# Performance work log

Measured on AMD Instinct MI355X. Metric: run time of the kernel, lower is better.

Reference implementation:

```python
import jax, jax.numpy as jnp
import numpy as np

MAX_LEVELS = 5
CHANNELS = 3


def _gauss_kernel(channels=CHANNELS):
    k = np.array([[1., 4., 6., 4., 1.],
                  [4., 16., 24., 16., 4.],
                  [6., 24., 36., 24., 6.],
                  [4., 16., 24., 16., 4.],
                  [1., 4., 6., 4., 1.]], dtype=np.float32) / 256.0
    return jnp.asarray(np.tile(k[None, None], (channels, 1, 1, 1)))  # (C,1,5,5)


def conv_gauss(img, kernel):
    # reflect-pad by 2 then depthwise 5x5 conv (groups = C)
    img = jnp.pad(img, ((0, 0), (0, 0), (2, 2), (2, 2)), mode='reflect')
    return jax.lax.conv_general_dilated(
        img, kernel, window_strides=(1, 1), padding='VALID',
        dimension_numbers=('NCHW', 'OIHW', 'NCHW'),
        feature_group_count=img.shape[1])


def downsample(x):
    return x[:, :, ::2, ::2]


def upsample(x, kernel):
    # zero-stuff: x at even (h,w) positions, zeros elsewhere, then smooth with 4*kernel
    b, c, h, w = x.shape
    up = jnp.zeros((b, c, 2 * h, 2 * w), dtype=x.dtype).at[:, :, ::2, ::2].set(x)
    return conv_gauss(up, 4.0 * kernel)


def laplacian_pyramid(img, kernel, max_levels=MAX_LEVELS):
    current = img
    pyr = []
    for _ in range(max_levels):
        filtered = conv_gauss(current, kernel)
        down = downsample(filtered)
        up = upsample(down, kernel)
        pyr.append(current - up)
        current = down
    return pyr


def setup_inputs() -> dict:
    key = jax.random.key(0)
    k1, k2 = jax.random.split(key)
    shape = (32, 3, 512, 512)
    return {
        'input': jax.random.normal(k1, shape, dtype=jnp.float32),
        'target': jax.random.normal(k2, shape, dtype=jnp.float32),
        'kernel': _gauss_kernel(CHANNELS),
    }


def reference(input, target, kernel):
    pyr_in = laplacian_pyramid(input, kernel, MAX_LEVELS)
    pyr_tg = laplacian_pyramid(target, kernel, MAX_LEVELS)
    # F.l1_loss default reduction: mean over all elements, per level
    return sum(jnp.mean(jnp.abs(a - b)) for a, b in zip(pyr_in, pyr_tg))
```

## Files before the change

kernel.cpp:

```cpp
#include <hip/hip_runtime.h>


#define BC 96
#define KA 0.0625f
#define KB 0.25f
#define KC 0.375f

__device__ __forceinline__ int refl(int i, int n) {
    if (i < 0) i = -i;
    if (i >= n) i = 2 * n - 2 - i;
    return i;
}

template<int H, int NC, bool DIFF>
__device__ __forceinline__ void load_raw(const float* __restrict__ pa,
                                         const float* __restrict__ pb,
                                         int r, int basec,
                                         float* __restrict__ a,
                                         float* __restrict__ b) {
    const int off = r * H + basec;
    if constexpr (NC == 8) {
        float4 a0 = *(const float4*)(pa + off);
        float4 a1 = *(const float4*)(pa + off + 4);
        a[0]=a0.x; a[1]=a0.y; a[2]=a0.z; a[3]=a0.w;
        a[4]=a1.x; a[5]=a1.y; a[6]=a1.z; a[7]=a1.w;
        if constexpr (DIFF) {
            float4 b0 = *(const float4*)(pb + off);
            float4 b1 = *(const float4*)(pb + off + 4);
            b[0]=b0.x; b[1]=b0.y; b[2]=b0.z; b[3]=b0.w;
            b[4]=b1.x; b[5]=b1.y; b[6]=b1.z; b[7]=b1.w;
        }
    } else if constexpr (NC == 4) {
        float4 a0 = *(const float4*)(pa + off);
        a[0]=a0.x; a[1]=a0.y; a[2]=a0.z; a[3]=a0.w;
        if constexpr (DIFF) {
            float4 b0 = *(const float4*)(pb + off);
            b[0]=b0.x; b[1]=b0.y; b[2]=b0.z; b[3]=b0.w;
        }
    } else {
        float2 a0 = *(const float2*)(pa + off);
        a[0]=a0.x; a[1]=a0.y;
        if constexpr (DIFF) {
            float2 b0 = *(const float2*)(pb + off);
            b[0]=b0.x; b[1]=b0.y;
        }
    }
}

template<int NC, bool DIFF>
__device__ __forceinline__ void materialize(const float* __restrict__ a,
                                            const float* __restrict__ b,
                                            float* __restrict__ c) {
#pragma unroll
    for (int i = 0; i < NC; ++i) c[i] = DIFF ? (a[i] - b[i]) : a[i];
}

template<int NC>
__device__ __forceinline__ void hconv(const float* __restrict__ c,
                                      float* __restrict__ o, int lane) {
    constexpr int ND = NC / 2;
    float e[NC + 3];
#pragma unroll
    for (int i = 0; i < NC; ++i) e[i + 2] = c[i];
    const bool l0 = (lane == 0), l63 = (lane == 63);
    { float v = __shfl(e[NC + 1], lane - 1); e[1] = l0 ? e[3] : v; }
    if constexpr (NC >= 4) {
        { float v = __shfl(e[NC], lane - 1); e[0] = l0 ? e[4] : v; }
        { float v = __shfl(e[2], lane + 1); e[NC + 2] = l63 ? e[NC] : v; }
    } else {
        e[0] = __shfl(e[2], l0 ? 1 : lane - 1);
        e[NC + 2] = __shfl(e[2], l63 ? 63 : lane + 1);
    }
#pragma unroll
    for (int j = 0; j < ND; ++j)
        o[j] = KA * e[2*j] + KB * e[2*j+1] + KC * e[2*j+2]
             + KB * e[2*j+3] + KA * e[2*j+4];
}

template<int H, int NC, bool DIFF, int R>
__global__ __launch_bounds__(256) void lap_slide(
        const float* __restrict__ A, const float* __restrict__ B,
        float* __restrict__ down, float* __restrict__ out, float invN) {
    constexpr int Hd = H / 2, ND = NC / 2, SPP = H / R;
    __shared__ float red[4];
    const int tid = threadIdx.x;
    const int lane = tid & 63, wid = tid >> 6;
    const int sid = blockIdx.x * 4 + wid;
    const int bc = sid / SPP;
    const int y0 = (sid % SPP) * R;
    const float* pa = A + (size_t)bc * H * H;
    const float* pb = DIFF ? (B + (size_t)bc * H * H) : nullptr;
    float* pd = down + (size_t)bc * Hd * Hd;
    const int basec = lane * NC;

    float h0[ND], h1[ND], h2[ND], h3[ND], h4[ND];
    float w0[NC], w1[NC], w2[NC];
    float eOld[NC], eMid[NC], oPrev[NC];
    float nA1[NC], nB1[NC], nA2[NC], nB2[NC];
    float c1[NC], c2[NC], t[NC], tb[NC];
#pragma unroll
    for (int i = 0; i < NC; ++i) {
        w0[i] = 0.f; w1[i] = 0.f; w2[i] = 0.f;
        eOld[i] = 0.f; oPrev[i] = 0.f;
    }
    float acc = 0.f;

    const int d0 = y0 >> 1;
    int dbeg = d0 - 1; if (dbeg < 0) dbeg = 0;
    const int dend = d0 + R / 2;

    load_raw<H,NC,DIFF>(pa, pb, refl(2*dbeg - 2, H), basec, t, tb);
    materialize<NC,DIFF>(t, tb, c1); hconv<NC>(c1, h0, lane);
    load_raw<H,NC,DIFF>(pa, pb, refl(2*dbeg - 1, H), basec, t, tb);
    materialize<NC,DIFF>(t, tb, c1); hconv<NC>(c1, h1, lane);
    load_raw<H,NC,DIFF>(pa, pb, refl(2*dbeg, H), basec, t, tb);
    materialize<NC,DIFF>(t, tb, eMid); hconv<NC>(eMid, h2, lane);
    load_raw<H,NC,DIFF>(pa, pb, refl(2*dbeg + 1, H), basec, nA1, nB1);
    load_raw<H,NC,DIFF>(pa, pb, refl(2*dbeg + 2, H), basec, nA2, nB2);

    for (int d = dbeg; d <= dend; ++d) {
        materialize<NC,DIFF>(nA1, nB1, c1);
        materialize<NC,DIFF>(nA2, nB2, c2);
        load_raw<H,NC,DIFF>(pa, pb, refl(2*d + 3, H), basec, nA1, nB1);
        load_raw<H,NC,DIFF>(pa, pb, refl(2*d + 4, H), basec, nA2, nB2);

        hconv<NC>(c1, h3, lane);
        hconv<NC>(c2, h4, lane);

        float dn[ND];
#pragma unroll
        for (int j = 0; j < ND; ++j)
            dn[j] = KA*h0[j] + KB*h1[j] + KC*h2[j] + KB*h3[j] + KA*h4[j];

        if (d >= d0 && d < d0 + R/2) {
            const int doff = d * Hd + lane * ND;
            if constexpr (ND == 4) {
                float4 s; s.x=dn[0]; s.y=dn[1]; s.z=dn[2]; s.w=dn[3];
                *(float4*)(pd + doff) = s;
            } else if constexpr (ND == 2) {
                float2 s; s.x=dn[0]; s.y=dn[1];
                *(float2*)(pd + doff) = s;
            } else {
                pd[doff] = dn[0];
            }
        }

        float dm, dp;
        if constexpr (ND >= 2) {
            { float v = __shfl(dn[ND-1], lane - 1); dm = (lane == 0)  ? dn[1]    : v; }
            { float v = __shfl(dn[0],    lane + 1); dp = (lane == 63) ? dn[ND-1] : v; }
        } else {
            dm = __shfl(dn[0], (lane == 0)  ? 1  : lane - 1);
            dp = __shfl(dn[0], (lane == 63) ? 63 : lane + 1);
        }
#pragma unroll
        for (int i = 0; i < NC; ++i) { w0[i] = w1[i]; w1[i] = w2[i]; }
#pragma unroll
        for (int j = 0; j < ND; ++j) {
            float lf = j ? dn[j-1] : dm;
            float rg = (j + 1 < ND) ? dn[j+1] : dp;
            w2[2*j]     = 0.125f * lf + 0.75f * dn[j] + 0.125f * rg;
            w2[2*j + 1] = 0.5f * (dn[j] + rg);
        }

        if (d >= d0 + 1) {
            const int ye = 2 * d - 2;
            if (ye == 0) {
#pragma unroll
                for (int i = 0; i < NC; ++i) {
                    acc += fabsf(eOld[i]  - (0.75f*w1[i] + 0.25f*w2[i]));
                    acc += fabsf(oPrev[i] - 0.5f*(w1[i] + w2[i]));
                }
            } else if (ye == H - 2) {
#pragma unroll
                for (int i = 0; i < NC; ++i) {
                    acc += fabsf(eOld[i]  - (0.125f*w0[i] + 0.875f*w1[i]));
                    acc += fabsf(oPrev[i] - w1[i]);
                }
            } else {
#pragma unroll
                for (int i = 0; i < NC; ++i) {
                    acc += fabsf(eOld[i]  - (0.125f*w0[i] + 0.75f*w1[i] + 0.125f*w2[i]));
                    acc += fabsf(oPrev[i] - 0.5f*(w1[i] + w2[i]));
                }
            }
        }

#pragma unroll
        for (int i = 0; i < NC; ++i) {
            eOld[i] = eMid[i]; eMid[i] = c2[i]; oPrev[i] = c1[i];
        }
#pragma unroll
        for (int j = 0; j < ND; ++j) { h0[j] = h2[j]; h1[j] = h3[j]; h2[j] = h4[j]; }
    }

#pragma unroll
    for (int off2 = 32; off2 > 0; off2 >>= 1)
        acc += __shfl_down(acc, off2, 64);
    if (lane == 0) red[wid] = acc;
    __syncthreads();
    if (tid == 0)
        atomicAdd(out, (red[0] + red[1] + red[2] + red[3]) * invN);
}

__global__ __launch_bounds__(1024) void lap_small(
        const float* __restrict__ dsrc, float* __restrict__ out,
        float invN3, float invN4) {
    __shared__ float p[64 * 66];
    __shared__ float hh[64 * 34];
    __shared__ float dd[32 * 34];
    __shared__ float W3[32 * 64];
    __shared__ float h4[32 * 18];
    __shared__ float d4[16 * 18];
    __shared__ float W4[16 * 32];
    __shared__ float red[16];
    const int tid = threadIdx.x;
    const float* src = dsrc + (size_t)blockIdx.x * 4096;
    for (int i = tid; i < 4096; i += 1024)
        p[(i >> 6) * 66 + (i & 63)] = src[i];
    __syncthreads();
    const float k[5] = {KA, KB, KC, KB, KA};
    for (int i = tid; i < 64 * 32; i += 1024) {
        int r = i >> 5, t = i & 31;
        const float* pr = p + r * 66;
        float s = 0.f;
#pragma unroll
        for (int v = 0; v < 5; ++v) s += k[v] * pr[refl(2*t + v - 2, 64)];
        hh[r * 34 + t] = s;
    }
    __syncthreads();
    for (int i = tid; i < 32 * 32; i += 1024) {
        int dy = i >> 5, t = i & 31;
        float s = 0.f;
#pragma unroll
        for (int u = 0; u < 5; ++u) s += k[u] * hh[refl(2*dy + u - 2, 64) * 34 + t];
        dd[dy * 34 + t] = s;
    }
    __syncthreads();
    for (int i = tid; i < 32 * 32; i += 1024) {
        int a = i >> 5, t = i & 31;
        const float* dr = dd + a * 34;
        float dm = dr[t == 0 ? 1 : t - 1];
        float dc = dr[t];
        float dp = dr[t == 31 ? 31 : t + 1];
        W3[a * 64 + 2*t]     = 0.125f * dm + 0.75f * dc + 0.125f * dp;
        W3[a * 64 + 2*t + 1] = 0.5f * (dc + dp);
    }
    __syncthreads();
    float acc3 = 0.f;
    for (int i = tid; i < 4096; i += 1024) {
        int y = i >> 6, x = i & 63;
        float cur = p[y * 66 + x];
        float up;
        if ((y & 1) == 0) {
            int a0 = refl(y - 2, 64) >> 1, a1 = y >> 1, a2 = refl(y + 2, 64) >> 1;
            up = 0.125f*W3[a0*64 + x] + 0.75f*W3[a1*64 + x] + 0.125f*W3[a2*64 + x];
        } else {
            int a0 = (y - 1) >> 1, a1 = refl(y + 1, 64) >> 1;
            up = 0.5f * (W3[a0*64 + x] + W3[a1*64 + x]);
        }
        acc3 += fabsf(cur - up);
    }
    __syncthreads();
    for (int i = tid; i < 32 * 16; i += 1024) {
        int r = i >> 4, t = i & 15;
        const float* pr = dd + r * 34;
        float s = 0.f;
#pragma unroll
        for (int v = 0; v < 5; ++v) s += k[v] * pr[refl(2*t + v - 2, 32)];
        h4[r * 18 + t] = s;
    }
    __syncthreads();
    for (int i = tid; i < 16 * 16; i += 1024) {
        int dy = i >> 4, t = i & 15;
        float s = 0.f;
#pragma unroll
        for (int u = 0; u < 5; ++u) s += k[u] * h4[refl(2*dy + u - 2, 32) * 18 + t];
        d4[dy * 18 + t] = s;
    }
    __syncthreads();
    for (int i = tid; i < 16 * 16; i += 1024) {
        int a = i >> 4, t = i & 15;
        const float* dr = d4 + a * 18;
        float dm = dr[t == 0 ? 1 : t - 1];
        float dc = dr[t];
        float dp = dr[t == 15 ? 15 : t + 1];
        W4[a * 32 + 2*t]     = 0.125f * dm + 0.75f * dc + 0.125f * dp;
        W4[a * 32 + 2*t + 1] = 0.5f * (dc + dp);
    }
    __syncthreads();
    float acc4 = 0.f;
    for (int i = tid; i < 1024; i += 1024) {
        int y = i >> 5, x = i & 31;
        float cur = dd[y * 34 + x];
        float up;
        if ((y & 1) == 0) {
            int a0 = refl(y - 2, 32) >> 1, a1 = y >> 1, a2 = refl(y + 2, 32) >> 1;
            up = 0.125f*W4[a0*32 + x] + 0.75f*W4[a1*32 + x] + 0.125f*W4[a2*32 + x];
        } else {
            int a0 = (y - 1) >> 1, a1 = refl(y + 1, 32) >> 1;
            up = 0.5f * (W4[a0*32 + x] + W4[a1*32 + x]);
        }
        acc4 += fabsf(cur - up);
    }
    float acc = acc3 * invN3 + acc4 * invN4;
#pragma unroll
    for (int off2 = 32; off2 > 0; off2 >>= 1)
        acc += __shfl_down(acc, off2, 64);
    int lane = tid & 63, wid = tid >> 6;
    if (lane == 0) red[wid] = acc;
    __syncthreads();
    if (tid == 0) {
        float s = 0.f;
#pragma unroll
        for (int i = 0; i < 16; ++i) s += red[i];
        atomicAdd(out, s);
    }
}

extern "C" void kernel_launch(void* const* d_in, const int* in_sizes, int n_in,
                              void* d_out, int out_size, void* d_ws, size_t ws_size,
                              hipStream_t stream) {
    const float* in = (const float*)d_in[0];
    const float* tg = (const float*)d_in[1];
    float* out = (float*)d_out;
    float* ws = (float*)d_ws;

    float* down0 = ws;
    float* down1 = down0 + (size_t)BC * 256 * 256;
    float* down2 = down1 + (size_t)BC * 128 * 128;

    hipMemsetAsync(out, 0, sizeof(float), stream);

    lap_slide<512, 8, true, 16><<<96 * 32 / 4, 256, 0, stream>>>(
        in, tg, down0, out, 1.f / (96.f * 512.f * 512.f));
    lap_slide<256, 4, false, 8><<<96 * 32 / 4, 256, 0, stream>>>(
        down0, nullptr, down1, out, 1.f / (96.f * 256.f * 256.f));
    lap_slide<128, 2, false, 4><<<96 * 32 / 4, 256, 0, stream>>>(
        down1, nullptr, down2, out, 1.f / (96.f * 128.f * 128.f));
    lap_small<<<BC, 1024, 0, stream>>>(
        down2, out, 1.f / (96.f * 64.f * 64.f), 1.f / (96.f * 32.f * 32.f));
}
```

Baseline: 263.4 us.

## Fold partial upsample terms into running residuals to cut registers; raise occupancy

The sliding-window state is restructured: instead of keeping three rows of horizontal upsample values plus the even/odd source rows, the kernel pre-subtracts each row's contribution into running residuals (pA, pB, pC), so fewer live arrays are carried between iterations. Launch bounds now request 8 blocks per CU, and the first level uses half the rows per wave with twice the grid. This aims to lower register pressure and raise occupancy and parallelism, at the cost of more halo reloads per strip and some reordering of floating-point sums.

New measurement: 522.2 us. +98.3%, slower.

```diff
diff --git a/kernel.cpp b/kernel.cpp
--- a/kernel.cpp
+++ b/kernel.cpp
@@ -78,7 +78,7 @@
 }
 
 template<int H, int NC, bool DIFF, int R>
-__global__ __launch_bounds__(256) void lap_slide(
+__global__ __launch_bounds__(256, 8) void lap_slide(
         const float* __restrict__ A, const float* __restrict__ B,
         float* __restrict__ down, float* __restrict__ out, float invN) {
     constexpr int Hd = H / 2, ND = NC / 2, SPP = H / R;
@@ -94,14 +94,12 @@
     const int basec = lane * NC;
 
     float h0[ND], h1[ND], h2[ND], h3[ND], h4[ND];
-    float w0[NC], w1[NC], w2[NC];
-    float eOld[NC], eMid[NC], oPrev[NC];
+    float wPrev[NC], pA[NC], pB[NC], pC[NC];
     float nA1[NC], nB1[NC], nA2[NC], nB2[NC];
     float c1[NC], c2[NC], t[NC], tb[NC];
 #pragma unroll
     for (int i = 0; i < NC; ++i) {
-        w0[i] = 0.f; w1[i] = 0.f; w2[i] = 0.f;
-        eOld[i] = 0.f; oPrev[i] = 0.f;
+        wPrev[i] = 0.f; pA[i] = 0.f; pB[i] = 0.f; pC[i] = 0.f;
     }
     float acc = 0.f;
 
@@ -114,7 +112,11 @@
     load_raw<H,NC,DIFF>(pa, pb, refl(2*dbeg - 1, H), basec, t, tb);
     materialize<NC,DIFF>(t, tb, c1); hconv<NC>(c1, h1, lane);
     load_raw<H,NC,DIFF>(pa, pb, refl(2*dbeg, H), basec, t, tb);
-    materialize<NC,DIFF>(t, tb, eMid); hconv<NC>(eMid, h2, lane);
+    materialize<NC,DIFF>(t, tb, c2); hconv<NC>(c2, h2, lane);
+    if (d0 == 0) {
+#pragma unroll
+        for (int i = 0; i < NC; ++i) pC[i] = c2[i];
+    }
     load_raw<H,NC,DIFF>(pa, pb, refl(2*dbeg + 1, H), basec, nA1, nB1);
     load_raw<H,NC,DIFF>(pa, pb, refl(2*dbeg + 2, H), basec, nA2, nB2);
 
@@ -153,14 +155,13 @@
             dm = __shfl(dn[0], (lane == 0)  ? 1  : lane - 1);
             dp = __shfl(dn[0], (lane == 63) ? 63 : lane + 1);
         }
-#pragma unroll
-        for (int i = 0; i < NC; ++i) { w0[i] = w1[i]; w1[i] = w2[i]; }
+        float wN[NC];
 #pragma unroll
         for (int j = 0; j < ND; ++j) {
             float lf = j ? dn[j-1] : dm;
             float rg = (j + 1 < ND) ? dn[j+1] : dp;
-            w2[2*j]     = 0.125f * lf + 0.75f * dn[j] + 0.125f * rg;
-            w2[2*j + 1] = 0.5f * (dn[j] + rg);
+            wN[2*j]     = 0.125f * lf + 0.75f * dn[j] + 0.125f * rg;
+            wN[2*j + 1] = 0.5f * (dn[j] + rg);
         }
 
         if (d >= d0 + 1) {
@@ -168,27 +169,30 @@
             if (ye == 0) {
 #pragma unroll
                 for (int i = 0; i < NC; ++i) {
-                    acc += fabsf(eOld[i]  - (0.75f*w1[i] + 0.25f*w2[i]));
-                    acc += fabsf(oPrev[i] - 0.5f*(w1[i] + w2[i]));
+                    acc += fabsf(pA[i] - (0.75f*wPrev[i] + 0.25f*wN[i]));
+                    acc += fabsf(pB[i] - 0.5f*wN[i]);
                 }
             } else if (ye == H - 2) {
 #pragma unroll
                 for (int i = 0; i < NC; ++i) {
-                    acc += fabsf(eOld[i]  - (0.125f*w0[i] + 0.875f*w1[i]));
-                    acc += fabsf(oPrev[i] - w1[i]);
+                    acc += fabsf(pA[i] - 0.875f*wPrev[i]);
+                    acc += fabsf(pB[i] - 0.5f*wPrev[i]);
                 }
             } else {
 #pragma unroll
                 for (int i = 0; i < NC; ++i) {
-                    acc += fabsf(eOld[i]  - (0.125f*w0[i] + 0.75f*w1[i] + 0.125f*w2[i]));
-                    acc += fabsf(oPrev[i] - 0.5f*(w1[i] + w2[i]));
+                    acc += fabsf(pA[i] - (0.75f*wPrev[i] + 0.125f*wN[i]));
+                    acc += fabsf(pB[i] - 0.5f*wN[i]);
                 }
             }
         }
 
 #pragma unroll
         for (int i = 0; i < NC; ++i) {
-            eOld[i] = eMid[i]; eMid[i] = c2[i]; oPrev[i] = c1[i];
+            pA[i] = pC[i];
+            pC[i] = c2[i] - 0.125f * wN[i];
+            pB[i] = c1[i] - 0.5f   * wN[i];
+            wPrev[i] = wN[i];
         }
 #pragma unroll
         for (int j = 0; j < ND; ++j) { h0[j] = h2[j]; h1[j] = h3[j]; h2[j] = h4[j]; }
@@ -332,7 +336,7 @@
 
     hipMemsetAsync(out, 0, sizeof(float), stream);
 
-    lap_slide<512, 8, true, 16><<<96 * 32 / 4, 256, 0, stream>>>(
+    lap_slide<512, 8, true, 8><<<96 * 64 / 4, 256, 0, stream>>>(
         in, tg, down0, out, 1.f / (96.f * 512.f * 512.f));
     lap_slide<256, 4, false, 8><<<96 * 32 / 4, 256, 0, stream>>>(
         down0, nullptr, down1, out, 1.f / (96.f * 256.f * 256.f));
```
